# Optimization experiments

Hardware: AMD Instinct MI355X
Metric: run time of the kernel (lower is better)

The kernel has to match this reference:

```python
import jax, jax.numpy as jnp
import numpy as np

D = 128
N_DRUG = 200000
N_PROT = 100000
E = 800000


def setup_inputs() -> dict:
    key = jax.random.key(0)
    ks = iter(jax.random.split(key, 64))
    inp = {}
    # initial node embeddings (nn.Embedding init: normal std=0.01)
    inp["x_drug"] = jax.random.normal(next(ks), (N_DRUG, D), jnp.float32) * 0.01
    inp["x_prot"] = jax.random.normal(next(ks), (N_PROT, D), jnp.float32) * 0.01
    # SAGEConv params per (layer, relation): lin_l (weight+bias), lin_r (weight, no bias)
    scale = 1.0 / np.sqrt(D)
    for l in (0, 1):
        for r in ("dp", "pd", "dd"):
            inp[f"Wl_{l}_{r}"] = jax.random.normal(next(ks), (D, D), jnp.float32) * scale
            inp[f"b_{l}_{r}"] = jnp.zeros((D,), jnp.float32)
            inp[f"Wr_{l}_{r}"] = jax.random.normal(next(ks), (D, D), jnp.float32) * scale
    # edge lists: (drug->protein), (protein->drug), (drug->drug)
    inp["e_dp_src"] = jax.random.randint(next(ks), (E,), 0, N_DRUG, dtype=jnp.int32)
    inp["e_dp_dst"] = jax.random.randint(next(ks), (E,), 0, N_PROT, dtype=jnp.int32)
    inp["e_pd_src"] = jax.random.randint(next(ks), (E,), 0, N_PROT, dtype=jnp.int32)
    inp["e_pd_dst"] = jax.random.randint(next(ks), (E,), 0, N_DRUG, dtype=jnp.int32)
    inp["e_dd_src"] = jax.random.randint(next(ks), (E,), 0, N_DRUG, dtype=jnp.int32)
    inp["e_dd_dst"] = jax.random.randint(next(ks), (E,), 0, N_DRUG, dtype=jnp.int32)
    return inp


def _sage(x_src, x_dst, src, dst, Wl, b, Wr):
    """PyG SAGEConv(aggr='mean'): lin_l(mean_neighbors) + lin_r(x_dst)."""
    n_dst = x_dst.shape[0]
    agg = jax.ops.segment_sum(x_src[src], dst, num_segments=n_dst)          # [n_dst, D]
    cnt = jax.ops.segment_sum(jnp.ones(src.shape, x_src.dtype), dst, num_segments=n_dst)
    mean = agg / jnp.maximum(cnt, 1.0)[:, None]  # isolated nodes -> 0
    return mean @ Wl.T + b + x_dst @ Wr.T


def _forward(xd, xp, params, edges):
    e_dp_s, e_dp_d, e_pd_s, e_pd_d, e_dd_s, e_dd_d = edges
    for l in (0, 1):
        p = params[l]
        # HeteroConv(aggr='sum'): sum SAGEConv outputs per destination node type
        new_p = _sage(xd, xp, e_dp_s, e_dp_d, *p["dp"])
        new_d = _sage(xp, xd, e_pd_s, e_pd_d, *p["pd"]) + _sage(xd, xd, e_dd_s, e_dd_d, *p["dd"])
        xd, xp = new_d, new_p
        if l == 0:  # relu (+ dropout as identity in eval) between layers only
            xd, xp = jax.nn.relu(xd), jax.nn.relu(xp)
    return jnp.concatenate([xd, xp], axis=0)  # [N_DRUG + N_PROT, D]


def reference(x_drug, x_prot,
              Wl_0_dp, b_0_dp, Wr_0_dp, Wl_0_pd, b_0_pd, Wr_0_pd, Wl_0_dd, b_0_dd, Wr_0_dd,
              Wl_1_dp, b_1_dp, Wr_1_dp, Wl_1_pd, b_1_pd, Wr_1_pd, Wl_1_dd, b_1_dd, Wr_1_dd,
              e_dp_src, e_dp_dst, e_pd_src, e_pd_dst, e_dd_src, e_dd_dst):
    params = [
        {"dp": (Wl_0_dp, b_0_dp, Wr_0_dp), "pd": (Wl_0_pd, b_0_pd, Wr_0_pd), "dd": (Wl_0_dd, b_0_dd, Wr_0_dd)},
        {"dp": (Wl_1_dp, b_1_dp, Wr_1_dp), "pd": (Wl_1_pd, b_1_pd, Wr_1_pd), "dd": (Wl_1_dd, b_1_dd, Wr_1_dd)},
    ]
    edges = (e_dp_src, e_dp_dst, e_pd_src, e_pd_dst, e_dd_src, e_dd_dst)
    return _forward(x_drug, x_prot, params, edges)
```

## Files before the change

### kernel.cpp

```cpp
#include <hip/hip_runtime.h>

#define D 128

using short8 = __attribute__((ext_vector_type(8))) short;
using f32x4 = __attribute__((ext_vector_type(4))) float;

__device__ inline unsigned short f2bf(float f) {
  unsigned u = __float_as_uint(f);
  u += 0x7fffu + ((u >> 16) & 1u);
  return (unsigned short)(u >> 16);
}

__device__ inline int swz(int r, int kbyte) {
  return ((r << 8) + kbyte) ^ ((r & 7) << 4);
}

__device__ inline unsigned relu_pk(unsigned w) {
  if (w & 0x8000u) w &= 0xffff0000u;
  if (w & 0x80000000u) w &= 0x0000ffffu;
  return w;
}


__global__ __launch_bounds__(256) void count_int_kernel(const int* __restrict__ dst,
                                                        int* __restrict__ cnt, int n) {
  int i = blockIdx.x * 256 + threadIdx.x;
  if (i < n) atomicAdd(&cnt[dst[i]], 1);
}

__global__ __launch_bounds__(256) void blocksum_kernel(const int* __restrict__ cnt,
                                                       int* __restrict__ bsums, int n) {
  __shared__ int sh[256];
  int i = blockIdx.x * 256 + threadIdx.x;
  sh[threadIdx.x] = (i < n) ? cnt[i] : 0;
  __syncthreads();
#pragma unroll
  for (int off = 128; off > 0; off >>= 1) {
    if (threadIdx.x < off) sh[threadIdx.x] += sh[threadIdx.x + off];
    __syncthreads();
  }
  if (threadIdx.x == 0) bsums[blockIdx.x] = sh[0];
}

__global__ __launch_bounds__(256) void scan_bsums_kernel(int* __restrict__ bsums, int nb) {
  __shared__ int sh[256];
  __shared__ int carry;
  if (threadIdx.x == 0) carry = 0;
  __syncthreads();
  for (int base = 0; base < nb; base += 256) {
    int i = base + threadIdx.x;
    int v = (i < nb) ? bsums[i] : 0;
    sh[threadIdx.x] = v;
    __syncthreads();
#pragma unroll
    for (int off = 1; off < 256; off <<= 1) {
      int t = (threadIdx.x >= off) ? sh[threadIdx.x - off] : 0;
      __syncthreads();
      sh[threadIdx.x] += t;
      __syncthreads();
    }
    int incl = sh[threadIdx.x];
    if (i < nb) bsums[i] = carry + incl - v;
    __syncthreads();
    if (threadIdx.x == 0) carry += sh[255];
    __syncthreads();
  }
}

__global__ __launch_bounds__(256) void scan_finalize_kernel(const int* __restrict__ cnt,
                                                            const int* __restrict__ bsums,
                                                            int* __restrict__ rowptr,
                                                            int n, int total) {
  __shared__ int sh[256];
  int i = blockIdx.x * 256 + threadIdx.x;
  int v = (i < n) ? cnt[i] : 0;
  sh[threadIdx.x] = v;
  __syncthreads();
#pragma unroll
  for (int off = 1; off < 256; off <<= 1) {
    int t = (threadIdx.x >= off) ? sh[threadIdx.x - off] : 0;
    __syncthreads();
    sh[threadIdx.x] += t;
    __syncthreads();
  }
  if (i < n) {
    rowptr[i] = bsums[blockIdx.x] + sh[threadIdx.x] - v;
    if (i == n - 1) rowptr[n] = total;
  }
}

__global__ __launch_bounds__(256) void fill_kernel(const int* __restrict__ src,
                                                   const int* __restrict__ dst,
                                                   int* __restrict__ cursor,
                                                   int* __restrict__ slots, int n) {
  int i = blockIdx.x * 256 + threadIdx.x;
  if (i < n) {
    int pos = atomicAdd(&cursor[dst[i]], 1);
    slots[pos] = src[i];
  }
}


__global__ __launch_bounds__(256) void prep_weights_kernel(
    const float* __restrict__ Wrpd, const float* __restrict__ Wrdd,
    const float* __restrict__ Wldd, const float* __restrict__ Wldp,
    const float* __restrict__ Wrdp, const float* __restrict__ Wlpd,
    const float* __restrict__ bpd, const float* __restrict__ bdd,
    unsigned short* __restrict__ Wb, float* __restrict__ bsum) {
  int i = blockIdx.x * 256 + threadIdx.x;
  const int M = D * D;
  if (i < M)           Wb[i] = f2bf(Wrpd[i] + Wrdd[i - 0 * M]);
  else if (i < 2 * M)  Wb[i] = f2bf(Wldd[i - 1 * M]);
  else if (i < 3 * M)  Wb[i] = f2bf(Wldp[i - 2 * M]);
  else if (i < 4 * M)  Wb[i] = f2bf(Wrdp[i - 3 * M]);
  else if (i < 5 * M)  Wb[i] = f2bf(Wlpd[i - 4 * M]);
  if (i < D) bsum[i] = bpd[i] + bdd[i];
}


template<typename XT, bool RELU>
__device__ inline short8 ld_frag(const XT* __restrict__ p, bool valid) {
  if constexpr (sizeof(XT) == 4) {
    float4 v0 = make_float4(0.f, 0.f, 0.f, 0.f), v1 = v0;
    if (valid) {
      v0 = *reinterpret_cast<const float4*>(p);
      v1 = *reinterpret_cast<const float4*>(p + 4);
    }
    if (RELU) {
      v0.x = fmaxf(v0.x, 0.f); v0.y = fmaxf(v0.y, 0.f);
      v0.z = fmaxf(v0.z, 0.f); v0.w = fmaxf(v0.w, 0.f);
      v1.x = fmaxf(v1.x, 0.f); v1.y = fmaxf(v1.y, 0.f);
      v1.z = fmaxf(v1.z, 0.f); v1.w = fmaxf(v1.w, 0.f);
    }
    short8 s;
    s[0] = (short)f2bf(v0.x); s[1] = (short)f2bf(v0.y);
    s[2] = (short)f2bf(v0.z); s[3] = (short)f2bf(v0.w);
    s[4] = (short)f2bf(v1.x); s[5] = (short)f2bf(v1.y);
    s[6] = (short)f2bf(v1.z); s[7] = (short)f2bf(v1.w);
    return s;
  } else {
    uint4 u = make_uint4(0, 0, 0, 0);
    if (valid) u = *reinterpret_cast<const uint4*>(p);
    if (RELU) { u.x = relu_pk(u.x); u.y = relu_pk(u.y); u.z = relu_pk(u.z); u.w = relu_pk(u.w); }
    union { uint4 u; short8 s; } cv; cv.u = u;
    return cv.s;
  }
}


template<typename XT, bool RELU, int NH, bool OUT0_BF16>
__global__ __launch_bounds__(256) void fused_gemm_kernel(
    const XT* __restrict__ X, const unsigned short* __restrict__ Wb,
    const float* __restrict__ bias0, void* __restrict__ out0,
    unsigned short* __restrict__ out1, unsigned short* __restrict__ out2,
    int nrows, int ntiles) {
  __shared__ short Wsh[NH * D * D];
  const int tid = threadIdx.x;

  for (int i = tid; i < NH * 4096; i += 256) {
    int mat = i >> 12;
    int idx = i & 4095;
    int r = idx >> 5;
    int kb = (idx & 31) * 8;
    ushort4 w = reinterpret_cast<const ushort4*>(Wb)[i];
    *reinterpret_cast<ushort4*>((char*)(Wsh + mat * D * D) + swz(r, kb)) = w;
  }
  __syncthreads();

  const int wv = tid >> 6, lane = tid & 63;
  const int l15 = lane & 15, lg = lane >> 4;

  float bias_c[8];
#pragma unroll
  for (int n = 0; n < 8; ++n) bias_c[n] = bias0[n * 16 + l15];

  for (int tile = blockIdx.x; tile < ntiles; tile += gridDim.x) {
    const size_t row0 = (size_t)tile * 128;
    const int limit = (int)min((long)128, (long)nrows - (long)row0);
    const int rA = wv * 32 + l15;

    short8 a[2][4];
    const bool full = (limit == 128);
#pragma unroll
    for (int t = 0; t < 4; ++t) {
      int k0 = t * 32 + lg * 8;
      a[0][t] = ld_frag<XT, RELU>(X + (row0 + rA) * D + k0, full || (rA < limit));
      a[1][t] = ld_frag<XT, RELU>(X + (row0 + rA + 16) * D + k0, full || (rA + 16 < limit));
    }

    f32x4 acc[NH][2][8] = {};
#pragma unroll
    for (int t = 0; t < 4; ++t) {
      const int kb = t * 64 + lg * 16;
#pragma unroll
      for (int h = 0; h < NH; ++h) {
        const char* base = (const char*)(Wsh + h * D * D);
#pragma unroll
        for (int n = 0; n < 8; ++n) {
          short8 b = *reinterpret_cast<const short8*>(base + swz(n * 16 + l15, kb));
          acc[h][0][n] = __builtin_amdgcn_mfma_f32_16x16x32_bf16(a[0][t], b, acc[h][0][n], 0, 0, 0);
          acc[h][1][n] = __builtin_amdgcn_mfma_f32_16x16x32_bf16(a[1][t], b, acc[h][1][n], 0, 0, 0);
        }
      }
    }

#pragma unroll
    for (int m = 0; m < 2; ++m) {
#pragma unroll
      for (int n = 0; n < 8; ++n) {
        const int col = n * 16 + l15;
#pragma unroll
        for (int r = 0; r < 4; ++r) {
          int lrow = wv * 32 + m * 16 + lg * 4 + r;
          if (lrow < limit) {
            size_t o = (row0 + lrow) * D + col;
            float v0 = acc[0][m][n][r] + bias_c[n];
            if (OUT0_BF16) reinterpret_cast<unsigned short*>(out0)[o] = f2bf(v0);
            else           reinterpret_cast<float*>(out0)[o] = v0;
            if (NH >= 2) out1[o] = f2bf(acc[1][m][n][r]);
            if (NH >= 3) out2[o] = f2bf(acc[2][m][n][r]);
          }
        }
      }
    }
  }
}


__device__ inline void addbf8(float* sum, uint4 v) {
  sum[0] += __uint_as_float(v.x << 16);
  sum[1] += __uint_as_float(v.x & 0xffff0000u);
  sum[2] += __uint_as_float(v.y << 16);
  sum[3] += __uint_as_float(v.y & 0xffff0000u);
  sum[4] += __uint_as_float(v.z << 16);
  sum[5] += __uint_as_float(v.z & 0xffff0000u);
  sum[6] += __uint_as_float(v.w << 16);
  sum[7] += __uint_as_float(v.w & 0xffff0000u);
}

__device__ inline float gather_one(const uint4* __restrict__ Y4,
                                   const int* __restrict__ rowptr,
                                   const int* __restrict__ slots,
                                   int node, int lane, float* sum) {
  int s0 = rowptr[node], s1 = rowptr[node + 1];
  for (int chunk = s0; chunk < s1; chunk += 16) {
    int idx = chunk + lane;
    int pre = (idx < s1) ? slots[idx] : 0;
    int m = s1 - chunk; if (m > 16) m = 16;
    int j = 0;
    for (; j + 4 <= m; j += 4) {
      int sA = __shfl(pre, j, 16);
      int sB = __shfl(pre, j + 1, 16);
      int sC = __shfl(pre, j + 2, 16);
      int sD = __shfl(pre, j + 3, 16);
      uint4 vA = Y4[(size_t)sA * 16 + lane];
      uint4 vB = Y4[(size_t)sB * 16 + lane];
      uint4 vC = Y4[(size_t)sC * 16 + lane];
      uint4 vD = Y4[(size_t)sD * 16 + lane];
      addbf8(sum, vA); addbf8(sum, vB); addbf8(sum, vC); addbf8(sum, vD);
    }
    for (; j < m; ++j) {
      int s = __shfl(pre, j, 16);
      addbf8(sum, Y4[(size_t)s * 16 + lane]);
    }
  }
  return 1.0f / fmaxf((float)(s1 - s0), 1.0f);
}

template<int NREL, bool ACC_BF16>
__global__ __launch_bounds__(256) void gatherN_kernel(
    const unsigned short* __restrict__ Y0, const int* __restrict__ rp0, const int* __restrict__ sl0,
    const unsigned short* __restrict__ Y1, const int* __restrict__ rp1, const int* __restrict__ sl1,
    void* __restrict__ acc, int nnodes) {
  long g = (long)blockIdx.x * 256 + threadIdx.x;
  int node = (int)(g >> 4);
  if (node >= nnodes) return;
  int lane = (int)(g & 15);

  float t0[8] = {}, t1[8] = {};
  float inv0 = gather_one(reinterpret_cast<const uint4*>(Y0), rp0, sl0, node, lane, t0);
  float inv1 = 0.f;
  if (NREL == 2)
    inv1 = gather_one(reinterpret_cast<const uint4*>(Y1), rp1, sl1, node, lane, t1);

  float a[8];
  if (ACC_BF16) {
    unsigned short* ap = (unsigned short*)acc + (size_t)node * D + lane * 8;
    uint4 u = *reinterpret_cast<uint4*>(ap);
    a[0] = __uint_as_float(u.x << 16); a[1] = __uint_as_float(u.x & 0xffff0000u);
    a[2] = __uint_as_float(u.y << 16); a[3] = __uint_as_float(u.y & 0xffff0000u);
    a[4] = __uint_as_float(u.z << 16); a[5] = __uint_as_float(u.z & 0xffff0000u);
    a[6] = __uint_as_float(u.w << 16); a[7] = __uint_as_float(u.w & 0xffff0000u);
#pragma unroll
    for (int i = 0; i < 8; ++i) {
      a[i] += t0[i] * inv0;
      if (NREL == 2) a[i] += t1[i] * inv1;
    }
    uint4 o;
    o.x = (unsigned)f2bf(a[0]) | ((unsigned)f2bf(a[1]) << 16);
    o.y = (unsigned)f2bf(a[2]) | ((unsigned)f2bf(a[3]) << 16);
    o.z = (unsigned)f2bf(a[4]) | ((unsigned)f2bf(a[5]) << 16);
    o.w = (unsigned)f2bf(a[6]) | ((unsigned)f2bf(a[7]) << 16);
    *reinterpret_cast<uint4*>(ap) = o;
  } else {
    float* ap = (float*)acc + (size_t)node * D + lane * 8;
    float4 a0 = *reinterpret_cast<float4*>(ap);
    float4 a1 = *reinterpret_cast<float4*>(ap + 4);
    a[0] = a0.x; a[1] = a0.y; a[2] = a0.z; a[3] = a0.w;
    a[4] = a1.x; a[5] = a1.y; a[6] = a1.z; a[7] = a1.w;
#pragma unroll
    for (int i = 0; i < 8; ++i) {
      a[i] += t0[i] * inv0;
      if (NREL == 2) a[i] += t1[i] * inv1;
    }
    *reinterpret_cast<float4*>(ap) = make_float4(a[0], a[1], a[2], a[3]);
    *reinterpret_cast<float4*>(ap + 4) = make_float4(a[4], a[5], a[6], a[7]);
  }
}


extern "C" void kernel_launch(void* const* d_in, const int* in_sizes, int n_in,
                              void* d_out, int out_size, void* d_ws, size_t ws_size,
                              hipStream_t stream) {
  const float* x_drug = (const float*)d_in[0];
  const float* x_prot = (const float*)d_in[1];
  const float* Wl0dp = (const float*)d_in[2];  const float* b0dp = (const float*)d_in[3];  const float* Wr0dp = (const float*)d_in[4];
  const float* Wl0pd = (const float*)d_in[5];  const float* b0pd = (const float*)d_in[6];  const float* Wr0pd = (const float*)d_in[7];
  const float* Wl0dd = (const float*)d_in[8];  const float* b0dd = (const float*)d_in[9];  const float* Wr0dd = (const float*)d_in[10];
  const float* Wl1dp = (const float*)d_in[11]; const float* b1dp = (const float*)d_in[12]; const float* Wr1dp = (const float*)d_in[13];
  const float* Wl1pd = (const float*)d_in[14]; const float* b1pd = (const float*)d_in[15]; const float* Wr1pd = (const float*)d_in[16];
  const float* Wl1dd = (const float*)d_in[17]; const float* b1dd = (const float*)d_in[18]; const float* Wr1dd = (const float*)d_in[19];
  const int* e_dp_s = (const int*)d_in[20]; const int* e_dp_d = (const int*)d_in[21];
  const int* e_pd_s = (const int*)d_in[22]; const int* e_pd_d = (const int*)d_in[23];
  const int* e_dd_s = (const int*)d_in[24]; const int* e_dd_d = (const int*)d_in[25];

  const int ND = in_sizes[0] / D;
  const int NP = in_sizes[1] / D;
  const int E_dp = in_sizes[20], E_pd = in_sizes[22], E_dd = in_sizes[24];

  unsigned short* accD  = (unsigned short*)d_ws;
  unsigned short* accP  = accD + (size_t)ND * D;
  unsigned short* bufdd = accP + (size_t)NP * D;
  unsigned short* bufdp = bufdd + (size_t)ND * D;
  unsigned short* bufpd = bufdp + (size_t)ND * D;
  unsigned short* Wb    = bufpd + (size_t)NP * D;
  float* bsum  = (float*)(Wb + 5 * D * D);
  int* rp_dp  = (int*)(bsum + D);
  int* rp_pd  = rp_dp + (NP + 2);
  int* rp_dd  = rp_pd + (ND + 2);
  int* sl_dp  = rp_dd + (ND + 2);
  int* sl_pd  = sl_dp + E_dp;
  int* sl_dd  = sl_pd + E_pd;
  int* cnt    = sl_dd + E_dd;
  int* bsums  = cnt + ND;

  auto cdiv = [](long a, long b) { return (int)((a + b - 1) / b); };

  auto build_csr = [&](const int* esrc, const int* edst, int ne, int ndst,
                       int* rowptr, int* slots) {
    int nb = cdiv(ndst, 256);
    hipMemsetAsync(cnt, 0, (size_t)ndst * sizeof(int), stream);
    count_int_kernel<<<cdiv(ne, 256), 256, 0, stream>>>(edst, cnt, ne);
    blocksum_kernel<<<nb, 256, 0, stream>>>(cnt, bsums, ndst);
    scan_bsums_kernel<<<1, 256, 0, stream>>>(bsums, nb);
    scan_finalize_kernel<<<nb, 256, 0, stream>>>(cnt, bsums, rowptr, ndst, ne);
    hipMemcpyAsync(cnt, rowptr, (size_t)ndst * sizeof(int), hipMemcpyDeviceToDevice, stream);
    fill_kernel<<<cdiv(ne, 256), 256, 0, stream>>>(esrc, edst, cnt, slots, ne);
  };

  build_csr(e_dp_s, e_dp_d, E_dp, NP, rp_dp, sl_dp);
  build_csr(e_pd_s, e_pd_d, E_pd, ND, rp_pd, sl_pd);
  build_csr(e_dd_s, e_dd_d, E_dd, ND, rp_dd, sl_dd);

  const int tilesD = cdiv(ND, 128), tilesP = cdiv(NP, 128);

  prep_weights_kernel<<<cdiv(5 * D * D, 256), 256, 0, stream>>>(
      Wr0pd, Wr0dd, Wl0dd, Wl0dp, Wr0dp, Wl0pd, b0pd, b0dd, Wb, bsum);
  fused_gemm_kernel<float, false, 3, true><<<256, 256, 0, stream>>>(
      x_drug, Wb, bsum, accD, bufdd, bufdp, ND, tilesD);
  fused_gemm_kernel<float, false, 2, true><<<512, 256, 0, stream>>>(
      x_prot, Wb + 3 * D * D, b0dp, accP, bufpd, nullptr, NP, tilesP);
  gatherN_kernel<2, true><<<cdiv((long)ND * 16, 256), 256, 0, stream>>>(
      bufpd, rp_pd, sl_pd, bufdd, rp_dd, sl_dd, accD, ND);
  gatherN_kernel<1, true><<<cdiv((long)NP * 16, 256), 256, 0, stream>>>(
      bufdp, rp_dp, sl_dp, nullptr, nullptr, nullptr, accP, NP);

  float* outD1 = (float*)d_out;
  float* outP1 = outD1 + (size_t)ND * D;
  prep_weights_kernel<<<cdiv(5 * D * D, 256), 256, 0, stream>>>(
      Wr1pd, Wr1dd, Wl1dd, Wl1dp, Wr1dp, Wl1pd, b1pd, b1dd, Wb, bsum);
  fused_gemm_kernel<unsigned short, true, 3, false><<<256, 256, 0, stream>>>(
      accD, Wb, bsum, outD1, bufdd, bufdp, ND, tilesD);
  fused_gemm_kernel<unsigned short, true, 2, false><<<512, 256, 0, stream>>>(
      accP, Wb + 3 * D * D, b1dp, outP1, bufpd, nullptr, NP, tilesP);
  gatherN_kernel<2, false><<<cdiv((long)ND * 16, 256), 256, 0, stream>>>(
      bufpd, rp_pd, sl_pd, bufdd, rp_dd, sl_dd, outD1, ND);
  gatherN_kernel<1, false><<<cdiv((long)NP * 16, 256), 256, 0, stream>>>(
      bufdp, rp_dp, sl_dp, nullptr, nullptr, nullptr, outP1, NP);
}
```

Baseline: 819.7 us.

## Permute output columns for vectorized bf16 stores and prefetch A tiles in GEMM

The weight prep now writes pre-swizzled bf16 weights, so the GEMM copies them into shared memory with plain 16-byte loads. In layer 0 it permutes the output columns so each lane owns eight contiguous columns and can write bf16 results as one uint4, and layer 1 inverts that permutation on its input. The GEMM moves to 512-thread blocks with 256-row tiles and double-buffers the A-fragment loads for the next tile. It also splits the three-head accumulation into two phases to cut register pressure. This trades simpler stores and overlapped loads for a cross-kernel column-permutation contract, which the layer-1 fp32 gather now follows with strided per-lane accesses.

After: 1.070 ms. 30.5% more time.

```diff
diff --git a/kernel.cpp b/kernel.cpp
--- a/kernel.cpp
+++ b/kernel.cpp
@@ -101,20 +101,39 @@
 }
 
 
+template<bool PERM>
 __global__ __launch_bounds__(256) void prep_weights_kernel(
     const float* __restrict__ Wrpd, const float* __restrict__ Wrdd,
     const float* __restrict__ Wldd, const float* __restrict__ Wldp,
     const float* __restrict__ Wrdp, const float* __restrict__ Wlpd,
     const float* __restrict__ bpd, const float* __restrict__ bdd,
     unsigned short* __restrict__ Wb, float* __restrict__ bsum) {
-  int i = blockIdx.x * 256 + threadIdx.x;
-  const int M = D * D;
-  if (i < M)           Wb[i] = f2bf(Wrpd[i] + Wrdd[i - 0 * M]);
-  else if (i < 2 * M)  Wb[i] = f2bf(Wldd[i - 1 * M]);
-  else if (i < 3 * M)  Wb[i] = f2bf(Wldp[i - 2 * M]);
-  else if (i < 4 * M)  Wb[i] = f2bf(Wrdp[i - 3 * M]);
-  else if (i < 5 * M)  Wb[i] = f2bf(Wlpd[i - 4 * M]);
-  if (i < D) bsum[i] = bpd[i] + bdd[i];
+  int g = blockIdx.x * 256 + threadIdx.x;
+  if (g < 5 * 4096) {
+    int mat = g >> 12, idx = g & 4095;
+    int c = idx >> 5, k4 = (idx & 31) * 4;
+    const float* src0;
+    const float* src1 = nullptr;
+    switch (mat) {
+      case 0: src0 = Wrpd; src1 = Wrdd; break;
+      case 1: src0 = Wldd; break;
+      case 2: src0 = Wldp; break;
+      case 3: src0 = Wrdp; break;
+      default: src0 = Wlpd; break;
+    }
+    unsigned short v[4];
+#pragma unroll
+    for (int j = 0; j < 4; ++j) {
+      int kp = k4 + j;
+      int kc = PERM ? ((kp & 7) * 16 + (kp >> 3)) : kp;
+      float f = src0[c * D + kc];
+      if (src1) f += src1[c * D + kc];
+      v[j] = f2bf(f);
+    }
+    *reinterpret_cast<ushort4*>((char*)(Wb + mat * D * D) + swz(c, k4 * 2)) =
+        make_ushort4(v[0], v[1], v[2], v[3]);
+  }
+  if (g < D) bsum[g] = bpd[g] + bdd[g];
 }
 
 
@@ -148,8 +167,8 @@
 }
 
 
-template<typename XT, bool RELU, int NH, bool OUT0_BF16>
-__global__ __launch_bounds__(256) void fused_gemm_kernel(
+template<typename XT, bool RELU, int NH, bool OUT0_F32>
+__global__ __launch_bounds__(512, 2) void fused_gemm_kernel(
     const XT* __restrict__ X, const unsigned short* __restrict__ Wb,
     const float* __restrict__ bias0, void* __restrict__ out0,
     unsigned short* __restrict__ out1, unsigned short* __restrict__ out2,
@@ -157,72 +176,125 @@
   __shared__ short Wsh[NH * D * D];
   const int tid = threadIdx.x;
 
-  for (int i = tid; i < NH * 4096; i += 256) {
-    int mat = i >> 12;
-    int idx = i & 4095;
-    int r = idx >> 5;
-    int kb = (idx & 31) * 8;
-    ushort4 w = reinterpret_cast<const ushort4*>(Wb)[i];
-    *reinterpret_cast<ushort4*>((char*)(Wsh + mat * D * D) + swz(r, kb)) = w;
-  }
+  for (int i = tid; i < NH * 2048; i += 512)
+    reinterpret_cast<uint4*>(Wsh)[i] = reinterpret_cast<const uint4*>(Wb)[i];
   __syncthreads();
 
   const int wv = tid >> 6, lane = tid & 63;
   const int l15 = lane & 15, lg = lane >> 4;
+  const int rbase = wv * 32;
 
   float bias_c[8];
 #pragma unroll
   for (int n = 0; n < 8; ++n) bias_c[n] = bias0[n * 16 + l15];
 
-  for (int tile = blockIdx.x; tile < ntiles; tile += gridDim.x) {
-    const size_t row0 = (size_t)tile * 128;
-    const int limit = (int)min((long)128, (long)nrows - (long)row0);
-    const int rA = wv * 32 + l15;
-
-    short8 a[2][4];
-    const bool full = (limit == 128);
+  auto loadA = [&](short8 (&a)[2][4], int tile) {
+    size_t row0 = (size_t)tile * 256;
+    long rem = (long)nrows - (long)row0;
+    int limit = (int)(rem < 256 ? rem : 256);
+    bool v0 = (rbase + l15) < limit, v1 = (rbase + l15 + 16) < limit;
+    const XT* b0 = X + (row0 + rbase + l15) * D;
+    const XT* b1 = X + (row0 + rbase + l15 + 16) * D;
 #pragma unroll
     for (int t = 0; t < 4; ++t) {
       int k0 = t * 32 + lg * 8;
-      a[0][t] = ld_frag<XT, RELU>(X + (row0 + rA) * D + k0, full || (rA < limit));
-      a[1][t] = ld_frag<XT, RELU>(X + (row0 + rA + 16) * D + k0, full || (rA + 16 < limit));
-    }
-
-    f32x4 acc[NH][2][8] = {};
-#pragma unroll
-    for (int t = 0; t < 4; ++t) {
-      const int kb = t * 64 + lg * 16;
-#pragma unroll
-      for (int h = 0; h < NH; ++h) {
-        const char* base = (const char*)(Wsh + h * D * D);
-#pragma unroll
-        for (int n = 0; n < 8; ++n) {
-          short8 b = *reinterpret_cast<const short8*>(base + swz(n * 16 + l15, kb));
-          acc[h][0][n] = __builtin_amdgcn_mfma_f32_16x16x32_bf16(a[0][t], b, acc[h][0][n], 0, 0, 0);
-          acc[h][1][n] = __builtin_amdgcn_mfma_f32_16x16x32_bf16(a[1][t], b, acc[h][1][n], 0, 0, 0);
+      a[0][t] = ld_frag<XT, RELU>(b0 + k0, v0);
+      a[1][t] = ld_frag<XT, RELU>(b1 + k0, v1);
+    }
+  };
+
+  auto store_bf16 = [&](f32x4 (&acc)[2][8], unsigned short* out, size_t row0,
+                        int limit, bool addb) {
+#pragma unroll
+    for (int m = 0; m < 2; ++m)
+#pragma unroll
+      for (int r = 0; r < 4; ++r) {
+        int lrow = rbase + m * 16 + lg * 4 + r;
+        if (lrow < limit) {
+          float f[8];
+#pragma unroll
+          for (int n = 0; n < 8; ++n) f[n] = acc[m][n][r] + (addb ? bias_c[n] : 0.f);
+          uint4 u;
+          u.x = (unsigned)f2bf(f[0]) | ((unsigned)f2bf(f[1]) << 16);
+          u.y = (unsigned)f2bf(f[2]) | ((unsigned)f2bf(f[3]) << 16);
+          u.z = (unsigned)f2bf(f[4]) | ((unsigned)f2bf(f[5]) << 16);
+          u.w = (unsigned)f2bf(f[6]) | ((unsigned)f2bf(f[7]) << 16);
+          *reinterpret_cast<uint4*>(out + (row0 + lrow) * D + l15 * 8) = u;
         }
       }
-    }
-
-#pragma unroll
-    for (int m = 0; m < 2; ++m) {
+  };
+
+  auto store_f32 = [&](f32x4 (&acc)[2][8], float* out, size_t row0, int limit) {
+#pragma unroll
+    for (int m = 0; m < 2; ++m)
 #pragma unroll
       for (int n = 0; n < 8; ++n) {
         const int col = n * 16 + l15;
 #pragma unroll
         for (int r = 0; r < 4; ++r) {
-          int lrow = wv * 32 + m * 16 + lg * 4 + r;
-          if (lrow < limit) {
-            size_t o = (row0 + lrow) * D + col;
-            float v0 = acc[0][m][n][r] + bias_c[n];
-            if (OUT0_BF16) reinterpret_cast<unsigned short*>(out0)[o] = f2bf(v0);
-            else           reinterpret_cast<float*>(out0)[o] = v0;
-            if (NH >= 2) out1[o] = f2bf(acc[1][m][n][r]);
-            if (NH >= 3) out2[o] = f2bf(acc[2][m][n][r]);
+          int lrow = rbase + m * 16 + lg * 4 + r;
+          if (lrow < limit) out[(row0 + lrow) * D + col] = acc[m][n][r] + bias_c[n];
+        }
+      }
+  };
+
+  auto do_tile = [&](short8 (&acur)[2][4], short8 (&anext)[2][4], int tile) {
+    int ntile = tile + (int)gridDim.x;
+    if (ntile < ntiles) loadA(anext, ntile);
+
+    size_t row0 = (size_t)tile * 256;
+    long rem = (long)nrows - (long)row0;
+    int limit = (int)(rem < 256 ? rem : 256);
+
+    constexpr int P1 = (NH >= 2) ? 2 : 1;
+    {
+      f32x4 acc[P1][2][8] = {};
+#pragma unroll
+      for (int t = 0; t < 4; ++t) {
+        const int kb = t * 64 + lg * 16;
+#pragma unroll
+        for (int h = 0; h < P1; ++h) {
+          const char* base = (const char*)(Wsh + h * D * D);
+#pragma unroll
+          for (int n = 0; n < 8; ++n) {
+            short8 b = *reinterpret_cast<const short8*>(base + swz(n * 16 + l15, kb));
+            acc[h][0][n] = __builtin_amdgcn_mfma_f32_16x16x32_bf16(acur[0][t], b, acc[h][0][n], 0, 0, 0);
+            acc[h][1][n] = __builtin_amdgcn_mfma_f32_16x16x32_bf16(acur[1][t], b, acc[h][1][n], 0, 0, 0);
           }
         }
       }
-    }
+      if (OUT0_F32) store_f32(acc[0], (float*)out0, row0, limit);
+      else          store_bf16(acc[0], (unsigned short*)out0, row0, limit, true);
+      if (P1 > 1)   store_bf16(acc[1], out1, row0, limit, false);
+    }
+    if constexpr (NH == 3) {
+      f32x4 acc2[2][8] = {};
+#pragma unroll
+      for (int t = 0; t < 4; ++t) {
+        const int kb = t * 64 + lg * 16;
+        const char* base = (const char*)(Wsh + 2 * D * D);
+#pragma unroll
+        for (int n = 0; n < 8; ++n) {
+          short8 b = *reinterpret_cast<const short8*>(base + swz(n * 16 + l15, kb));
+          acc2[0][n] = __builtin_amdgcn_mfma_f32_16x16x32_bf16(acur[0][t], b, acc2[0][n], 0, 0, 0);
+          acc2[1][n] = __builtin_amdgcn_mfma_f32_16x16x32_bf16(acur[1][t], b, acc2[1][n], 0, 0, 0);
+        }
+      }
+      store_bf16(acc2, out2, row0, limit, false);
+    }
+  };
+
+  short8 aA[2][4], aB[2][4];
+  int tile = blockIdx.x;
+  if (tile >= ntiles) return;
+  loadA(aA, tile);
+  while (true) {
+    do_tile(aA, aB, tile);
+    tile += gridDim.x;
+    if (tile >= ntiles) break;
+    do_tile(aB, aA, tile);
+    tile += gridDim.x;
+    if (tile >= ntiles) break;
   }
 }
 
@@ -267,7 +339,7 @@
   return 1.0f / fmaxf((float)(s1 - s0), 1.0f);
 }
 
-template<int NREL, bool ACC_BF16>
+template<int NREL, int MODE>
 __global__ __launch_bounds__(256) void gatherN_kernel(
     const unsigned short* __restrict__ Y0, const int* __restrict__ rp0, const int* __restrict__ sl0,
     const unsigned short* __restrict__ Y1, const int* __restrict__ rp1, const int* __restrict__ sl1,
@@ -283,10 +355,10 @@
   if (NREL == 2)
     inv1 = gather_one(reinterpret_cast<const uint4*>(Y1), rp1, sl1, node, lane, t1);
 
-  float a[8];
-  if (ACC_BF16) {
+  if (MODE == 1) {
     unsigned short* ap = (unsigned short*)acc + (size_t)node * D + lane * 8;
     uint4 u = *reinterpret_cast<uint4*>(ap);
+    float a[8];
     a[0] = __uint_as_float(u.x << 16); a[1] = __uint_as_float(u.x & 0xffff0000u);
     a[2] = __uint_as_float(u.y << 16); a[3] = __uint_as_float(u.y & 0xffff0000u);
     a[4] = __uint_as_float(u.z << 16); a[5] = __uint_as_float(u.z & 0xffff0000u);
@@ -303,18 +375,14 @@
     o.w = (unsigned)f2bf(a[6]) | ((unsigned)f2bf(a[7]) << 16);
     *reinterpret_cast<uint4*>(ap) = o;
   } else {
-    float* ap = (float*)acc + (size_t)node * D + lane * 8;
-    float4 a0 = *reinterpret_cast<float4*>(ap);
-    float4 a1 = *reinterpret_cast<float4*>(ap + 4);
-    a[0] = a0.x; a[1] = a0.y; a[2] = a0.z; a[3] = a0.w;
-    a[4] = a1.x; a[5] = a1.y; a[6] = a1.z; a[7] = a1.w;
+    float* ap = (float*)acc + (size_t)node * D + lane;
 #pragma unroll
     for (int i = 0; i < 8; ++i) {
-      a[i] += t0[i] * inv0;
-      if (NREL == 2) a[i] += t1[i] * inv1;
-    }
-    *reinterpret_cast<float4*>(ap) = make_float4(a[0], a[1], a[2], a[3]);
-    *reinterpret_cast<float4*>(ap + 4) = make_float4(a[4], a[5], a[6], a[7]);
+      float a = ap[i * 16];
+      a += t0[i] * inv0;
+      if (NREL == 2) a += t1[i] * inv1;
+      ap[i * 16] = a;
+    }
   }
 }
 
@@ -372,29 +440,29 @@
   build_csr(e_pd_s, e_pd_d, E_pd, ND, rp_pd, sl_pd);
   build_csr(e_dd_s, e_dd_d, E_dd, ND, rp_dd, sl_dd);
 
-  const int tilesD = cdiv(ND, 128), tilesP = cdiv(NP, 128);
-
-  prep_weights_kernel<<<cdiv(5 * D * D, 256), 256, 0, stream>>>(
+  const int tilesD = cdiv(ND, 256), tilesP = cdiv(NP, 256);
+
+  prep_weights_kernel<false><<<80, 256, 0, stream>>>(
       Wr0pd, Wr0dd, Wl0dd, Wl0dp, Wr0dp, Wl0pd, b0pd, b0dd, Wb, bsum);
-  fused_gemm_kernel<float, false, 3, true><<<256, 256, 0, stream>>>(
+  fused_gemm_kernel<float, false, 3, false><<<256, 512, 0, stream>>>(
       x_drug, Wb, bsum, accD, bufdd, bufdp, ND, tilesD);
-  fused_gemm_kernel<float, false, 2, true><<<512, 256, 0, stream>>>(
+  fused_gemm_kernel<float, false, 2, false><<<256, 512, 0, stream>>>(
       x_prot, Wb + 3 * D * D, b0dp, accP, bufpd, nullptr, NP, tilesP);
-  gatherN_kernel<2, true><<<cdiv((long)ND * 16, 256), 256, 0, stream>>>(
+  gatherN_kernel<2, 1><<<cdiv((long)ND * 16, 256), 256, 0, stream>>>(
       bufpd, rp_pd, sl_pd, bufdd, rp_dd, sl_dd, accD, ND);
-  gatherN_kernel<1, true><<<cdiv((long)NP * 16, 256), 256, 0, stream>>>(
+  gatherN_kernel<1, 1><<<cdiv((long)NP * 16, 256), 256, 0, stream>>>(
       bufdp, rp_dp, sl_dp, nullptr, nullptr, nullptr, accP, NP);
 
   float* outD1 = (float*)d_out;
   float* outP1 = outD1 + (size_t)ND * D;
-  prep_weights_kernel<<<cdiv(5 * D * D, 256), 256, 0, stream>>>(
+  prep_weights_kernel<true><<<80, 256, 0, stream>>>(
       Wr1pd, Wr1dd, Wl1dd, Wl1dp, Wr1dp, Wl1pd, b1pd, b1dd, Wb, bsum);
-  fused_gemm_kernel<unsigned short, true, 3, false><<<256, 256, 0, stream>>>(
+  fused_gemm_kernel<unsigned short, true, 3, true><<<256, 512, 0, stream>>>(
       accD, Wb, bsum, outD1, bufdd, bufdp, ND, tilesD);
-  fused_gemm_kernel<unsigned short, true, 2, false><<<512, 256, 0, stream>>>(
+  fused_gemm_kernel<unsigned short, true, 2, true><<<256, 512, 0, stream>>>(
       accP, Wb + 3 * D * D, b1dp, outP1, bufpd, nullptr, NP, tilesP);
-  gatherN_kernel<2, false><<<cdiv((long)ND * 16, 256), 256, 0, stream>>>(
+  gatherN_kernel<2, 0><<<cdiv((long)ND * 16, 256), 256, 0, stream>>>(
       bufpd, rp_pd, sl_pd, bufdd, rp_dd, sl_dd, outD1, ND);
-  gatherN_kernel<1, false><<<cdiv((long)NP * 16, 256), 256, 0, stream>>>(
+  gatherN_kernel<1, 0><<<cdiv((long)NP * 16, 256), 256, 0, stream>>>(
       bufdp, rp_dp, sl_dp, nullptr, nullptr, nullptr, outP1, NP);
 }
```
